# Optimization experiments

Measured on AMD Instinct MI355X. Metric: run time of the kernel, lower is better.

## Reference

```python
import jax, jax.numpy as jnp
import numpy as np

B, S, T = 256, 512, 20
VOCAB, E, H, SKIP = 100000, 25, 128, 64


def _lstm_scan(x, skip, mask, K, R, Sk, b):
    # x:[S,B,E], skip:[S,B,SKIP], mask:[S,B] bool. Keras RNN mask semantics:
    # masked steps carry previous h/c and emit previous h.
    Bn = x.shape[1]
    Hn = R.shape[0]
    def step(carry, inp):
        h, c = carry
        xt, st, mt = inp
        z = xt @ K + h @ R + st @ Sk + b            # [B,4H]
        zi, zf, zg, zo = jnp.split(z, 4, axis=-1)
        cn = jax.nn.sigmoid(zf) * c + jax.nn.sigmoid(zi) * jnp.tanh(zg)
        hn = jax.nn.sigmoid(zo) * jnp.tanh(cn)
        m = mt[:, None]
        h2 = jnp.where(m, hn, h)
        c2 = jnp.where(m, cn, c)
        return (h2, c2), h2
    init = (jnp.zeros((Bn, Hn), x.dtype), jnp.zeros((Bn, Hn), x.dtype))
    (hF, cF), hs = jax.lax.scan(step, init, (x, skip, mask))
    return hs, hF


def setup_inputs() -> dict:
    key = jax.random.key(0)
    ks = jax.random.split(key, 20)
    p = lambda k, shp: jax.random.normal(k, shp, dtype=jnp.float32) * 0.05
    inp = {
        "input_tags": jax.random.randint(ks[0], (B, S, T), 0, VOCAB, dtype=jnp.int32),
        "embedded_skips": jax.random.normal(ks[1], (B, S, SKIP), dtype=jnp.float32),
        "emb_table": p(ks[2], (VOCAB, E)),
        "kernel_f": p(ks[3], (E, 4 * H)),
        "rec_f": p(ks[4], (H, 4 * H)),
        "skip_f": p(ks[5], (SKIP, 4 * H)),
        "bias_f": jnp.zeros((4 * H,), jnp.float32),
        "kernel_b": p(ks[6], (E, 4 * H)),
        "rec_b": p(ks[7], (H, 4 * H)),
        "skip_b": p(ks[8], (SKIP, 4 * H)),
        "bias_b": jnp.zeros((4 * H,), jnp.float32),
        "Wk": p(ks[9], (2 * H, H)),
        "bk": jnp.zeros((H,), jnp.float32),
        "Wq": p(ks[10], (H, H)),
        "bq": jnp.zeros((H,), jnp.float32),
        "We": p(ks[11], (H, 1)),
        "be": jnp.zeros((1,), jnp.float32),
    }
    return inp


def reference(input_tags, embedded_skips, emb_table,
              kernel_f, rec_f, skip_f, bias_f,
              kernel_b, rec_b, skip_b, bias_b,
              Wk, bk, Wq, bq, We, be):
    mask3 = input_tags != 0                          # [B,S,T]
    emb = emb_table[input_tags]                      # [B,S,T,E]
    num_mask = mask3.astype(emb.dtype)
    summed = jnp.sum(emb * num_mask[..., None], axis=2)   # [B,S,E]
    denom = jnp.sum(num_mask, axis=2)                     # [B,S]
    denom = jnp.where(denom == 0, jnp.ones_like(denom), denom)
    gru_inp = summed / denom[..., None]                   # [B,S,E]
    step_mask = mask3[:, :, 0]                            # [B,S]

    # time-major for scan
    x_t = jnp.swapaxes(gru_inp, 0, 1)
    s_t = jnp.swapaxes(embedded_skips, 0, 1)
    m_t = jnp.swapaxes(step_mask, 0, 1)

    hs_f, h_fwd = _lstm_scan(x_t, s_t, m_t, kernel_f, rec_f, skip_f, bias_f)
    hs_b_rev, _ = _lstm_scan(x_t[::-1], s_t[::-1], m_t[::-1], kernel_b, rec_b, skip_b, bias_b)
    hs_b = hs_b_rev[::-1]
    out = jnp.swapaxes(jnp.concatenate([hs_f, hs_b], axis=-1), 0, 1)  # [B,S,2H]

    keys = out @ Wk + bk                                  # [B,S,H]
    queries = (h_fwd @ Wq + bq)[:, None, :]               # [B,1,H]
    energy = jnp.tanh(keys + queries) @ We + be           # [B,S,1]
    energy = energy + (1.0 - step_mask.astype(energy.dtype))[..., None] * -1e9
    weights = jax.nn.softmax(energy, axis=1)
    context = jnp.sum(weights * out, axis=1)              # [B,2H]
    return context
```

## Files before the change

### kernel.cpp

```cpp
#include <hip/hip_runtime.h>
#include <math.h>

#define Bb 256
#define Ss 512
#define Tt 20
#define Ee 25
#define Hh 128
#define SKIPn 64
#define H4n 512
#define BSn (Bb*Ss)
#define MG 4
#define HP 160
#define ZP 516
#define AP 264
#define LOG2E 1.4426950408889634f

typedef _Float16 f16x8 __attribute__((ext_vector_type(8)));
typedef _Float16 f16x4 __attribute__((ext_vector_type(4)));
typedef float f32x4 __attribute__((ext_vector_type(4)));

__device__ __forceinline__ float rcpf(float x) { return __builtin_amdgcn_rcpf(x); }
__device__ __forceinline__ float exp2f_(float x) { return __builtin_amdgcn_exp2f(x); }

__device__ __forceinline__ void lgkm_barrier() {
    __asm__ __volatile__("" ::: "memory");
    __builtin_amdgcn_s_waitcnt(0xC07F);
    __builtin_amdgcn_s_barrier();
    __asm__ __volatile__("" ::: "memory");
}

#define POOL_BLOCKS (BSn / 8)
#define CVT_BLOCKS  (BSn * SKIPn / (256 * 8))
__global__ void __launch_bounds__(256)
prep_kernel(const int* __restrict__ tags, const float* __restrict__ table,
            const float* __restrict__ skips,
            _Float16* __restrict__ gru16, float* __restrict__ maskf,
            float* __restrict__ maskt, _Float16* __restrict__ sk16) {
    if (blockIdx.x >= POOL_BLOCKS) {
        size_t i = ((size_t)(blockIdx.x - POOL_BLOCKS) * 256 + threadIdx.x) * 8;
        f32x4 a = *(const f32x4*)(skips + i);
        f32x4 b = *(const f32x4*)(skips + i + 4);
        f16x8 o;
#pragma unroll
        for (int j = 0; j < 4; j++) { o[j] = (_Float16)a[j]; o[j + 4] = (_Float16)b[j]; }
        *(f16x8*)(sk16 + i) = o;
        return;
    }
    int group = blockIdx.x * 8 + (threadIdx.x >> 5);
    int lane = threadIdx.x & 31;
    int b = group >> 9;
    int t = group & (Ss - 1);
    const int* tg = tags + (size_t)group * Tt;
    const int el = (lane < Ee) ? lane : (Ee - 1);

    int tagv[Tt];
#pragma unroll
    for (int tt = 0; tt < Tt; tt++) tagv[tt] = tg[tt];

    float vv[Tt];
#pragma unroll
    for (int tt = 0; tt < Tt; tt++)
        vv[tt] = table[(size_t)tagv[tt] * Ee + el];

    float acc = 0.0f;
    int cnt = 0;
#pragma unroll
    for (int tt = 0; tt < Tt; tt++) {
        const bool nz = (tagv[tt] != 0);
        cnt += nz ? 1 : 0;
        acc += nz ? vv[tt] : 0.0f;
    }
    float scale = rcpf((float)(cnt > 0 ? cnt : 1));
    float v = (lane < Ee) ? acc * scale : 0.0f;
    gru16[((size_t)t * Bb + b) * 32 + lane] = (_Float16)v;
    if (lane == 0) {
        float m = (tagv[0] != 0) ? 1.0f : 0.0f;
        maskf[group] = m;
        maskt[(size_t)t * Bb + b] = m;
    }
}

__global__ void __launch_bounds__(512)
__attribute__((amdgpu_waves_per_eu(2, 2)))
scan_kernel(const _Float16* __restrict__ gru16, const _Float16* __restrict__ sk16,
            const float* __restrict__ maskt,
            const float* __restrict__ Kf, const float* __restrict__ Rf,
            const float* __restrict__ Skf, const float* __restrict__ bf,
            const float* __restrict__ Kb, const float* __restrict__ Rb,
            const float* __restrict__ Skb, const float* __restrict__ bb,
            _Float16* __restrict__ hs16, float* __restrict__ hfwd)
{
    __shared__ __align__(16) _Float16 h16[2 * MG * HP];
    __shared__ __align__(16) _Float16 zlds[2][16 * 4 * ZP];

    const int tid = threadIdx.x;
    const int lane = tid & 63;
    const int w = tid >> 6;
    const int l16 = lane & 15;
    const int q = lane >> 4;
    const int mb = l16 >> 2;
    const int bg = blockIdx.x & 63;
    const int dir = blockIdx.x >> 6;
    const int b0 = bg * MG;
    const int col = 16 * w + l16;

    const float* Kw = dir ? Kb : Kf;
    const float* Rw = dir ? Rb : Rf;
    const float* Sw = dir ? Skb : Skf;
    const float* bw = dir ? bb : bf;
    const float gs[4] = {LOG2E, LOG2E, 2.0f * LOG2E, LOG2E};

    f16x8 hfr[4][4];
#pragma unroll
    for (int kt = 0; kt < 4; kt++) {
#pragma unroll
        for (int g = 0; g < 4; g++) {
            const int n = g * Hh + col;
            f16x8 v;
#pragma unroll
            for (int j = 0; j < 8; j++)
                v[j] = (_Float16)(Rw[(32 * kt + 8 * q + j) * H4n + n] * gs[g]);
            hfr[kt][g] = v;
        }
    }
    f16x8 bx[4], bs0[4], bs1[4];
    f32x4 biasA[4];
#pragma unroll
    for (int g = 0; g < 4; g++) {
        const int n = g * Hh + col;
        f16x8 vx, v0, v1;
#pragma unroll
        for (int j = 0; j < 8; j++) {
            const int kk = 8 * q + j;
            vx[j] = (_Float16)(((kk < Ee) ? Kw[kk * H4n + n] : 0.0f) * gs[g]);
            v0[j] = (_Float16)(Sw[kk * H4n + n] * gs[g]);
            v1[j] = (_Float16)(Sw[(32 + kk) * H4n + n] * gs[g]);
        }
        bx[g] = vx; bs0[g] = v0; bs1[g] = v1;
        const float bv = bw[g * Hh + col] * gs[g];
        f32x4 ba = {bv, bv, bv, bv};
        biasA[g] = ba;
    }
    const f32x4 zacc4 = {0.0f, 0.0f, 0.0f, 0.0f};

    for (int idx = tid; idx < 2 * MG * HP; idx += 512) h16[idx] = (_Float16)0.0f;

    float c = 0.0f, h = 0.0f;

    const int tsub = l16 >> 2, bbn = l16 & 3;
    const int tg0 = dir ? (Ss - 1 - tsub) : tsub;
    const _Float16* px = gru16 + ((size_t)tg0 * Bb + b0 + bbn) * 32 + 8 * q;
    const _Float16* ps = sk16 + ((size_t)(b0 + bbn) * Ss + tg0) * SKIPn + 8 * q;
    ptrdiff_t pxd = (dir ? -4 : 4) * (ptrdiff_t)(Bb * 32);
    ptrdiff_t psd = (dir ? -4 : 4) * (ptrdiff_t)SKIPn;

    const float* mpf = maskt + (size_t)(dir ? (Ss - 1) : 0) * Bb + b0 + q;
    const ptrdiff_t mdelta = dir ? -(ptrdiff_t)Bb : (ptrdiff_t)Bb;
    float mreg[2];
    mreg[0] = mpf[0]; mreg[1] = mpf[mdelta];
    mpf += 2 * mdelta;

    _Float16* hsp = hs16 + ((size_t)(b0 + q) * Ss + (dir ? Ss - 1 : 0)) * (2 * Hh)
                    + dir * Hh + col;
    const ptrdiff_t odelta = dir ? -(2 * Hh) : (2 * Hh);

    f16x8 gx, g0, g1;
    auto ldA = [&]() {
        gx = *(const f16x8*)px;
        g0 = *(const f16x8*)ps;
        g1 = *(const f16x8*)(ps + 32);
        px += pxd; ps += psd;
    };

    f32x4 zc[4];

    ldA();
#pragma unroll
    for (int T = 0; T < 4; T++) {
        const f16x8 ax = gx, a0 = g0, a1 = g1;
        ldA();
#pragma unroll
        for (int g = 0; g < 4; g++) {
            zc[g] = __builtin_amdgcn_mfma_f32_16x16x32_f16(ax, bx[g],  biasA[g], 0, 0, 0);
            zc[g] = __builtin_amdgcn_mfma_f32_16x16x32_f16(a0, bs0[g], zc[g], 0, 0, 0);
            zc[g] = __builtin_amdgcn_mfma_f32_16x16x32_f16(a1, bs1[g], zc[g], 0, 0, 0);
        }
        _Float16* zw = &zlds[0][0] + ((4 * T + q) * 4) * ZP + col * 4;
#pragma unroll
        for (int r = 0; r < 4; r++) {
            f16x4 o;
            o[0] = (_Float16)zc[0][r]; o[1] = (_Float16)zc[1][r];
            o[2] = (_Float16)zc[2][r]; o[3] = (_Float16)zc[3][r];
            *(f16x4*)(zw + r * ZP) = o;
        }
    }
    __syncthreads();

#pragma unroll 1
    for (int k = 0; k < 32; ++k) {
        const _Float16* zr = &zlds[k & 1][0];
        _Float16* zwb = &zlds[(k + 1) & 1][0];

#pragma unroll
        for (int j = 0; j < 16; ++j) {
            const int T = j >> 2, ph = j & 3;

            const _Float16* hb = h16 + (j & 1) * (MG * HP);
            const f16x8 ah0 = *(const f16x8*)(hb + mb * HP +  0 + 8 * q);
            const f16x8 ah1 = *(const f16x8*)(hb + mb * HP + 32 + 8 * q);
            const f16x8 ah2 = *(const f16x8*)(hb + mb * HP + 64 + 8 * q);
            const f16x8 ah3 = *(const f16x8*)(hb + mb * HP + 96 + 8 * q);
            const f16x4 z4 = *(const f16x4*)(zr + (j * 4 + q) * ZP + col * 4);

            f32x4 accA[4], accB[4];
#pragma unroll
            for (int g = 0; g < 4; g++) {
                accA[g] = __builtin_amdgcn_mfma_f32_16x16x32_f16(ah0, hfr[0][g], zacc4, 0, 0, 0);
                accB[g] = __builtin_amdgcn_mfma_f32_16x16x32_f16(ah1, hfr[1][g], zacc4, 0, 0, 0);
                accA[g] = __builtin_amdgcn_mfma_f32_16x16x32_f16(ah2, hfr[2][g], accA[g], 0, 0, 0);
                accB[g] = __builtin_amdgcn_mfma_f32_16x16x32_f16(ah3, hfr[3][g], accB[g], 0, 0, 0);
            }

            if (ph == 0) {
#pragma unroll
                for (int g = 0; g < 4; g++)
                    zc[g] = __builtin_amdgcn_mfma_f32_16x16x32_f16(gx, bx[g], biasA[g], 0, 0, 0);
            } else if (ph == 1) {
#pragma unroll
                for (int g = 0; g < 4; g++)
                    zc[g] = __builtin_amdgcn_mfma_f32_16x16x32_f16(g0, bs0[g], zc[g], 0, 0, 0);
            } else if (ph == 2) {
#pragma unroll
                for (int g = 0; g < 4; g++)
                    zc[g] = __builtin_amdgcn_mfma_f32_16x16x32_f16(g1, bs1[g], zc[g], 0, 0, 0);
                if (j == 10 && k == 30) { pxd = 0; psd = 0; }
                ldA();
            } else {
                _Float16* zw = zwb + ((4 * T + q) * 4) * ZP + col * 4;
#pragma unroll
                for (int r = 0; r < 4; r++) {
                    f16x4 o;
                    o[0] = (_Float16)zc[0][r]; o[1] = (_Float16)zc[1][r];
                    o[2] = (_Float16)zc[2][r]; o[3] = (_Float16)zc[3][r];
                    *(f16x4*)(zw + r * ZP) = o;
                }
            }

            const float mk = mreg[j & 1];
            mreg[j & 1] = *mpf; mpf += mdelta;
            const float zi = accA[0][0] + accB[0][0] + (float)z4[0];
            const float zf = accA[1][0] + accB[1][0] + (float)z4[1];
            const float zg = accA[2][0] + accB[2][0] + (float)z4[2];
            const float zo = accA[3][0] + accB[3][0] + (float)z4[3];
            const float ei = exp2f_(-zi);
            const float ef = exp2f_(-zf);
            const float eg = exp2f_(-zg);
            const float eo = exp2f_(-zo);
            const float pi = 1.0f + ei, pg = 1.0f + eg, pf = 1.0f + ef;
            const float p  = pi * pg;
            const float t1 = (1.0f - eg) * pf;
            const float cn = fmaf(c, p, t1) * rcpf(pf * p);
            const float ec = exp2f_(cn * (-2.0f * LOG2E));
            const float hn = (1.0f - ec) * rcpf((1.0f + eo) * (1.0f + ec));
            const bool mm = (mk != 0.0f);
            c = mm ? cn : c;
            h = mm ? hn : h;

            _Float16* hw = h16 + ((j + 1) & 1) * (MG * HP);
            hw[q * HP + col] = (_Float16)h;
            *hsp = (_Float16)h;
            hsp += odelta;
            lgkm_barrier();
        }
    }

    if (dir == 0) hfwd[(size_t)(b0 + q) * Hh + col] = h;
}

__global__ void __launch_bounds__(512)
attn_kernel(const _Float16* __restrict__ hs16, const float* __restrict__ hfwd,
            const float* __restrict__ Wq, const float* __restrict__ bq,
            const float* __restrict__ bk,
            const float* __restrict__ Wk, const float* __restrict__ We,
            const float* __restrict__ maskf, float* __restrict__ outp)
{
    __shared__ float hfl[Hh];
    __shared__ float qpart[4][Hh];
    __shared__ float qtot_s[Hh];
    __shared__ float epart[8][16];
    __shared__ float psh[16];
    __shared__ float mls[Ss];
    __shared__ float dls[16];
    __shared__ float ctxp[16][2 * Hh + 1];
    __shared__ __align__(16) _Float16 atile[2][16 * AP];

    const int tid = threadIdx.x;
    const int lane = tid & 63;
    const int w = tid >> 6;
    const int l16 = lane & 15;
    const int q = lane >> 4;
    const int b = blockIdx.x;
    const int j = 16 * w + l16;
    const int seg = tid >> 5;
    const int cg = tid & 31;

    f16x8 bk16[8];
#pragma unroll
    for (int kt = 0; kt < 8; kt++) {
        f16x8 v;
#pragma unroll
        for (int jj = 0; jj < 8; jj++)
            v[jj] = (_Float16)Wk[(32 * kt + 8 * q + jj) * Hh + j];
        bk16[kt] = v;
    }
    const float wej = We[j];

    mls[tid] = maskf[(size_t)b * Ss + tid];
    if (tid < Hh) hfl[tid] = hfwd[(size_t)b * Hh + tid];
    __syncthreads();
    {
        const int jj = tid & 127, sg = tid >> 7;
        float p = 0.0f;
#pragma unroll
        for (int k = 0; k < 32; k++)
            p += hfl[32 * sg + k] * Wq[(32 * sg + k) * Hh + jj];
        qpart[sg][jj] = p;
    }
    __syncthreads();
    if (tid < Hh)
        qtot_s[tid] = qpart[0][tid] + qpart[1][tid] + qpart[2][tid] + qpart[3][tid]
                      + bq[tid] + bk[tid];
    __syncthreads();
    const float qj = qtot_s[j];

    const _Float16* hb = hs16 + (size_t)b * Ss * (2 * Hh);
    *(f16x8*)(&atile[0][seg * AP + cg * 8]) =
        *(const f16x8*)(hb + (size_t)seg * (2 * Hh) + cg * 8);
    float ctxa[8];
#pragma unroll
    for (int jj = 0; jj < 8; jj++) ctxa[jj] = 0.0f;
    float dsum = 0.0f;
    __syncthreads();

#pragma unroll 1
    for (int st = 0; st < 32; st++) {
        const int p = st & 1;
        f16x8 sreg;
        if (st < 31)
            sreg = *(const f16x8*)(hb + (size_t)((st + 1) * 16 + seg) * (2 * Hh) + cg * 8);

        f32x4 acc0 = {0.f, 0.f, 0.f, 0.f}, acc1 = {0.f, 0.f, 0.f, 0.f};
#pragma unroll
        for (int kt = 0; kt < 4; kt++) {
            const f16x8 a = *(const f16x8*)(&atile[p][l16 * AP + kt * 32 + 8 * q]);
            acc0 = __builtin_amdgcn_mfma_f32_16x16x32_f16(a, bk16[kt], acc0, 0, 0, 0);
        }
#pragma unroll
        for (int kt = 4; kt < 8; kt++) {
            const f16x8 a = *(const f16x8*)(&atile[p][l16 * AP + kt * 32 + 8 * q]);
            acc1 = __builtin_amdgcn_mfma_f32_16x16x32_f16(a, bk16[kt], acc1, 0, 0, 0);
        }
        float vals[4];
#pragma unroll
        for (int r = 0; r < 4; r++) {
            const float x = acc0[r] + acc1[r] + qj;
            const float e = exp2f_(fminf(x * (-2.0f * LOG2E), 80.0f));
            vals[r] = (1.0f - e) * rcpf(1.0f + e) * wej;
        }
#pragma unroll
        for (int m = 1; m < 16; m <<= 1) {
#pragma unroll
            for (int r = 0; r < 4; r++) vals[r] += __shfl_xor(vals[r], m);
        }
        if (l16 == 0) {
#pragma unroll
            for (int r = 0; r < 4; r++) epart[w][4 * q + r] = vals[r];
        }
        __syncthreads();
        if (tid < 16) {
            float e = epart[0][tid] + epart[1][tid] + epart[2][tid] + epart[3][tid]
                    + epart[4][tid] + epart[5][tid] + epart[6][tid] + epart[7][tid];
            psh[tid] = mls[st * 16 + tid] * exp2f_(e * LOG2E);
        }
        __syncthreads();
        {
            const float wv = psh[seg];
            const f16x8 hv = *(const f16x8*)(&atile[p][seg * AP + cg * 8]);
#pragma unroll
            for (int jj = 0; jj < 8; jj++) ctxa[jj] = fmaf(wv, (float)hv[jj], ctxa[jj]);
            dsum += wv;
        }
        if (st < 31)
            *(f16x8*)(&atile[p ^ 1][seg * AP + cg * 8]) = sreg;
        __syncthreads();
    }

#pragma unroll
    for (int jj = 0; jj < 8; jj++) ctxp[seg][8 * cg + jj] = ctxa[jj];
    if (cg == 0) dls[seg] = dsum;
    __syncthreads();
    if (tid < 2 * Hh) {
        float s = 0.0f;
#pragma unroll
        for (int sg = 0; sg < 16; sg++) s += ctxp[sg][tid];
        float d = 0.0f;
#pragma unroll
        for (int sg = 0; sg < 16; sg++) d += dls[sg];
        outp[(size_t)b * (2 * Hh) + tid] = s * rcpf(d);
    }
}

extern "C" void kernel_launch(void* const* d_in, const int* in_sizes, int n_in,
                              void* d_out, int out_size, void* d_ws, size_t ws_size,
                              hipStream_t stream) {
    const int*   tags  = (const int*)d_in[0];
    const float* skips = (const float*)d_in[1];
    const float* table = (const float*)d_in[2];
    const float* Kf    = (const float*)d_in[3];
    const float* Rf    = (const float*)d_in[4];
    const float* Skf   = (const float*)d_in[5];
    const float* bf    = (const float*)d_in[6];
    const float* Kb    = (const float*)d_in[7];
    const float* Rb    = (const float*)d_in[8];
    const float* Skb   = (const float*)d_in[9];
    const float* bb    = (const float*)d_in[10];
    const float* Wk    = (const float*)d_in[11];
    const float* bk    = (const float*)d_in[12];
    const float* Wq    = (const float*)d_in[13];
    const float* bq    = (const float*)d_in[14];
    const float* We    = (const float*)d_in[15];

    char* ws = (char*)d_ws;
    _Float16* gru16 = (_Float16*)ws; ws += (size_t)BSn * 32 * 2;
    _Float16* sk16  = (_Float16*)ws; ws += (size_t)BSn * SKIPn * 2;
    float* maskf = (float*)ws; ws += (size_t)BSn * 4;
    float* maskt_base = (float*)ws; ws += ((size_t)BSn + 4 * Bb) * 4;
    float* maskt = maskt_base + 2 * Bb;
    _Float16* hs16 = (_Float16*)ws; ws += (size_t)BSn * 2 * Hh * 2;
    float* hfwd  = (float*)ws; ws += (size_t)Bb * Hh * 4;

    prep_kernel<<<POOL_BLOCKS + CVT_BLOCKS, 256, 0, stream>>>(
        tags, table, skips, gru16, maskf, maskt, sk16);
    scan_kernel<<<128, 512, 0, stream>>>(gru16, sk16, maskt,
                                         Kf, Rf, Skf, bf,
                                         Kb, Rb, Skb, bb,
                                         hs16, hfwd);
    attn_kernel<<<Bb, 512, 0, stream>>>(hs16, hfwd, Wq, bq, bk, Wk, We, maskf,
                                        (float*)d_out);
}
```

Before: 466.9 us.

## Process 64 timesteps per attention iteration and drop the extra barrier

The attention kernel now stages 64 sequence rows per iteration instead of 16, running 4 MFMA tiles per k-step and cutting the loop from 32 to 8 iterations. The energy reduction across waves is now done redundantly by every thread reading epart directly, which removes the psh stage and one __syncthreads per iteration. The intent is to lower barrier and loop overhead and expose more MFMA parallelism. The cost is higher shared memory use (a larger atile), more registers for the prefetch and accumulators, and a redundant 8-way sum in each thread.

```diff
diff --git a/kernel.cpp b/kernel.cpp
--- a/kernel.cpp
+++ b/kernel.cpp
@@ -287,12 +287,11 @@
     __shared__ float hfl[Hh];
     __shared__ float qpart[4][Hh];
     __shared__ float qtot_s[Hh];
-    __shared__ float epart[8][16];
-    __shared__ float psh[16];
+    __shared__ float epart[8][64];
     __shared__ float mls[Ss];
     __shared__ float dls[16];
     __shared__ float ctxp[16][2 * Hh + 1];
-    __shared__ __align__(16) _Float16 atile[2][16 * AP];
+    __shared__ __align__(16) _Float16 atile[2][64 * AP];
 
     const int tid = threadIdx.x;
     const int lane = tid & 63;
@@ -334,8 +333,10 @@
     const float qj = qtot_s[j];
 
     const _Float16* hb = hs16 + (size_t)b * Ss * (2 * Hh);
-    *(f16x8*)(&atile[0][seg * AP + cg * 8]) =
-        *(const f16x8*)(hb + (size_t)seg * (2 * Hh) + cg * 8);
+#pragma unroll
+    for (int t = 0; t < 4; t++)
+        *(f16x8*)(&atile[0][(seg + 16 * t) * AP + cg * 8]) =
+            *(const f16x8*)(hb + (size_t)(seg + 16 * t) * (2 * Hh) + cg * 8);
     float ctxa[8];
 #pragma unroll
     for (int jj = 0; jj < 8; jj++) ctxa[jj] = 0.0f;
@@ -343,55 +344,80 @@
     __syncthreads();
 
 #pragma unroll 1
-    for (int st = 0; st < 32; st++) {
+    for (int st = 0; st < 8; st++) {
         const int p = st & 1;
-        f16x8 sreg;
-        if (st < 31)
-            sreg = *(const f16x8*)(hb + (size_t)((st + 1) * 16 + seg) * (2 * Hh) + cg * 8);
-
-        f32x4 acc0 = {0.f, 0.f, 0.f, 0.f}, acc1 = {0.f, 0.f, 0.f, 0.f};
+        f16x8 sreg[4];
+        if (st < 7) {
+#pragma unroll
+            for (int t = 0; t < 4; t++)
+                sreg[t] = *(const f16x8*)(hb + (size_t)((st + 1) * 64 + seg + 16 * t) * (2 * Hh) + cg * 8);
+        }
+
+        f32x4 ta[4], tb[4];
+#pragma unroll
+        for (int t = 0; t < 4; t++) {
+            f32x4 z = {0.f, 0.f, 0.f, 0.f};
+            ta[t] = z; tb[t] = z;
+        }
 #pragma unroll
         for (int kt = 0; kt < 4; kt++) {
-            const f16x8 a = *(const f16x8*)(&atile[p][l16 * AP + kt * 32 + 8 * q]);
-            acc0 = __builtin_amdgcn_mfma_f32_16x16x32_f16(a, bk16[kt], acc0, 0, 0, 0);
+#pragma unroll
+            for (int t = 0; t < 4; t++) {
+                const f16x8 a = *(const f16x8*)(&atile[p][(16 * t + l16) * AP + kt * 32 + 8 * q]);
+                ta[t] = __builtin_amdgcn_mfma_f32_16x16x32_f16(a, bk16[kt], ta[t], 0, 0, 0);
+            }
         }
 #pragma unroll
         for (int kt = 4; kt < 8; kt++) {
-            const f16x8 a = *(const f16x8*)(&atile[p][l16 * AP + kt * 32 + 8 * q]);
-            acc1 = __builtin_amdgcn_mfma_f32_16x16x32_f16(a, bk16[kt], acc1, 0, 0, 0);
-        }
-        float vals[4];
-#pragma unroll
-        for (int r = 0; r < 4; r++) {
-            const float x = acc0[r] + acc1[r] + qj;
-            const float e = exp2f_(fminf(x * (-2.0f * LOG2E), 80.0f));
-            vals[r] = (1.0f - e) * rcpf(1.0f + e) * wej;
+#pragma unroll
+            for (int t = 0; t < 4; t++) {
+                const f16x8 a = *(const f16x8*)(&atile[p][(16 * t + l16) * AP + kt * 32 + 8 * q]);
+                tb[t] = __builtin_amdgcn_mfma_f32_16x16x32_f16(a, bk16[kt], tb[t], 0, 0, 0);
+            }
+        }
+        float vals[16];
+#pragma unroll
+        for (int t = 0; t < 4; t++) {
+#pragma unroll
+            for (int r = 0; r < 4; r++) {
+                const float x = ta[t][r] + tb[t][r] + qj;
+                const float e = exp2f_(fminf(x * (-2.0f * LOG2E), 80.0f));
+                vals[4 * t + r] = (1.0f - e) * rcpf(1.0f + e) * wej;
+            }
         }
 #pragma unroll
         for (int m = 1; m < 16; m <<= 1) {
 #pragma unroll
-            for (int r = 0; r < 4; r++) vals[r] += __shfl_xor(vals[r], m);
+            for (int r = 0; r < 16; r++) vals[r] += __shfl_xor(vals[r], m);
         }
         if (l16 == 0) {
 #pragma unroll
-            for (int r = 0; r < 4; r++) epart[w][4 * q + r] = vals[r];
+            for (int t = 0; t < 4; t++)
+#pragma unroll
+                for (int r = 0; r < 4; r++)
+                    epart[w][16 * t + 4 * q + r] = vals[4 * t + r];
         }
         __syncthreads();
-        if (tid < 16) {
-            float e = epart[0][tid] + epart[1][tid] + epart[2][tid] + epart[3][tid]
-                    + epart[4][tid] + epart[5][tid] + epart[6][tid] + epart[7][tid];
-            psh[tid] = mls[st * 16 + tid] * exp2f_(e * LOG2E);
-        }
-        __syncthreads();
+
         {
-            const float wv = psh[seg];
-            const f16x8 hv = *(const f16x8*)(&atile[p][seg * AP + cg * 8]);
-#pragma unroll
-            for (int jj = 0; jj < 8; jj++) ctxa[jj] = fmaf(wv, (float)hv[jj], ctxa[jj]);
-            dsum += wv;
-        }
-        if (st < 31)
-            *(f16x8*)(&atile[p ^ 1][seg * AP + cg * 8]) = sreg;
+#pragma unroll
+            for (int t = 0; t < 4; t++) {
+                const int row = seg + 16 * t;
+                float e = epart[0][row];
+#pragma unroll
+                for (int ww = 1; ww < 8; ww++) e += epart[ww][row];
+                const float pv = mls[st * 64 + row] * exp2f_(e * LOG2E);
+                const f16x8 hv = *(const f16x8*)(&atile[p][row * AP + cg * 8]);
+#pragma unroll
+                for (int jj = 0; jj < 8; jj++) ctxa[jj] = fmaf(pv, (float)hv[jj], ctxa[jj]);
+                dsum += pv;
+            }
+        }
+        if (st < 7) {
+#pragma unroll
+            for (int t = 0; t < 4; t++)
+                *(f16x8*)(&atile[p ^ 1][(seg + 16 * t) * AP + cg * 8]) = sreg[t];
+        }
         __syncthreads();
     }
 
```

Measured after the change: 454.9 us. -2.6%, faster.
